# Performance work log

Measured on AMD Instinct MI355X. Metric: run time of the kernel, lower is better.

The kernel has to match this reference:

```python
import jax, jax.numpy as jnp
import numpy as np

B, L, K = 4, 1536, 30
NUM_RBF = 16
NUM_POS = 16
EDGE_F = 128
MAX_REL = 32
EDGE_IN = NUM_POS + NUM_RBF * 9 + 7  # 167
LN_EPS = 1e-5


def _norml(x):
    # F.normalize with a grad-safe epsilon
    return x * jax.lax.rsqrt(jnp.sum(x * x, -1, keepdims=True) + 1e-12)


def _gather_nodes(nodes, idx):
    # nodes [B,L,C], idx [B,L,K] -> [B,L,K,C]
    b = jnp.arange(nodes.shape[0])[:, None, None]
    return nodes[b, idx]


def _rbf(D):
    mu = jnp.linspace(2.0, 22.0, NUM_RBF)
    sigma = (22.0 - 2.0) / NUM_RBF
    return jnp.exp(-(((D[..., None] - mu) / sigma) ** 2))


def _get_rbf(A, Bc, E_idx):
    D = jnp.sqrt(jnp.sum((A[:, :, None, :] - Bc[:, None, :, :]) ** 2, -1) + 1e-6)
    Dn = jnp.take_along_axis(D, E_idx, axis=2)
    return _rbf(Dn)


def _quaternions(R):
    # R [B,L,K,3,3] -> Q [B,L,K,4]
    diag = jnp.diagonal(R, axis1=-2, axis2=-1)
    Rxx, Ryy, Rzz = diag[..., 0], diag[..., 1], diag[..., 2]
    mags = 0.5 * jnp.sqrt(jnp.abs(1.0 + jnp.stack(
        [Rxx - Ryy - Rzz, -Rxx + Ryy - Rzz, -Rxx - Ryy + Rzz], -1)) + 1e-12)
    signs = jnp.sign(jnp.stack(
        [R[..., 2, 1] - R[..., 1, 2],
         R[..., 0, 2] - R[..., 2, 0],
         R[..., 1, 0] - R[..., 0, 1]], -1))
    xyz = signs * mags
    w = jnp.sqrt(jax.nn.relu(1.0 + diag.sum(-1, keepdims=True)) + 1e-12) / 2.0
    return _norml(jnp.concatenate([xyz, w], -1))


def _orientations_coarse(X, E_idx, eps=1e-6):
    dX = X[:, 1:] - X[:, :-1]                              # [B,L-1,3]
    dn = jnp.sqrt(jnp.sum(dX * dX, -1) + 1e-12)
    band = ((dn > 3.6) & (dn < 4.0)).astype(X.dtype)
    U = _norml(dX * band[..., None])
    u2, u1, u0 = U[:, :-2], U[:, 1:-1], U[:, 2:]
    n2 = _norml(jnp.cross(u2, u1))
    n1 = _norml(jnp.cross(u1, u0))
    cosA = jnp.clip(-(u1 * u0).sum(-1), -1 + eps, 1 - eps)
    A = jnp.arccos(cosA)
    cosD = jnp.clip((n2 * n1).sum(-1), -1 + eps, 1 - eps)
    Dang = jnp.sign((u2 * n1).sum(-1)) * jnp.arccos(cosD)
    AD = jnp.stack([jnp.cos(A), jnp.sin(A) * jnp.cos(Dang), jnp.sin(A) * jnp.sin(Dang)], 2)
    AD = jnp.pad(AD, ((0, 0), (1, 2), (0, 0)))
    o1 = _norml(u2 - u1)
    O = jnp.stack([o1, n2, jnp.cross(o1, n2)], 2).reshape(X.shape[0], -1, 9)
    O = jnp.pad(O, ((0, 0), (1, 2), (0, 0)))                # [B,L,9]
    On = _gather_nodes(O, E_idx).reshape(E_idx.shape + (3, 3))
    Xn = _gather_nodes(X, E_idx)
    O = O.reshape(X.shape[0], -1, 3, 3)
    dXk = Xn - X[:, :, None, :]                             # [B,L,K,3]
    dU = _norml(jnp.einsum('blij,blkj->blki', O, dXk))
    R = jnp.einsum('blji,blkjm->blkim', O, On)
    Q = _quaternions(R)
    return AD, jnp.concatenate([dU, Q], -1)                 # O_features [B,L,K,7]


def _forward(Ca, mask, residue_idx, chain_labels, W_pos, b_pos, W_edge, gamma_e, beta_e):
    # KNN graph: pairwise distances + smallest-k
    m2 = mask[:, :, None] * mask[:, None, :]
    dX = Ca[:, None, :, :] - Ca[:, :, None, :]
    D = m2 * jnp.sqrt(jnp.sum(dX * dX, -1) + 1e-6)
    Dmax = jnp.max(D, -1, keepdims=True)
    Dadj = D + (1.0 - m2) * Dmax
    neg, E_idx = jax.lax.top_k(-Dadj, K)
    D_neighbors = -neg

    Ca0 = jnp.pad(Ca[:, :-1], ((0, 0), (1, 0), (0, 0)))
    Ca2 = jnp.pad(Ca[:, 1:], ((0, 0), (0, 1), (0, 0)))
    _, O_features = _orientations_coarse(Ca, E_idx)

    RBF_all = jnp.concatenate([
        _rbf(D_neighbors),
        _get_rbf(Ca0, Ca0, E_idx), _get_rbf(Ca2, Ca2, E_idx),
        _get_rbf(Ca0, Ca, E_idx), _get_rbf(Ca0, Ca2, E_idx),
        _get_rbf(Ca, Ca0, E_idx), _get_rbf(Ca, Ca2, E_idx),
        _get_rbf(Ca2, Ca0, E_idx), _get_rbf(Ca2, Ca, E_idx)], -1)

    offset = residue_idx[:, :, None] - residue_idx[:, None, :]
    offset = jnp.take_along_axis(offset, E_idx, axis=2)
    dch = (chain_labels[:, :, None] == chain_labels[:, None, :]).astype(jnp.int32)
    Ech = jnp.take_along_axis(dch, E_idx, axis=2)
    d = jnp.clip(offset + MAX_REL, 0, 2 * MAX_REL) * Ech + (1 - Ech) * (2 * MAX_REL + 1)
    E_pos = W_pos.T[d] + b_pos                              # one_hot @ W^T as row gather

    E = jnp.concatenate([E_pos, RBF_all, O_features], -1)   # [B,L,K,167]
    E = E @ W_edge.T                                        # [B,L,K,128]
    mu = E.mean(-1, keepdims=True)
    var = E.var(-1, keepdims=True)
    E = (E - mu) * jax.lax.rsqrt(var + LN_EPS) * gamma_e + beta_e
    return E, E_idx


def setup_inputs():
    key = jax.random.key(0)
    ks = jax.random.split(key, 3)
    Ca = 3.0 * jax.random.normal(ks[0], (B, L, 3), jnp.float32)
    mask = jnp.ones((B, L), jnp.float32)
    residue_idx = (jnp.arange(B * L, dtype=jnp.int32).reshape(B, L)) % L
    chain_labels = jnp.zeros((B, L), jnp.int32)
    W_pos = 0.05 * jax.random.normal(ks[1], (NUM_POS, 2 * MAX_REL + 2), jnp.float32)
    b_pos = jnp.zeros((NUM_POS,), jnp.float32)
    W_edge = 0.05 * jax.random.normal(ks[2], (EDGE_F, EDGE_IN), jnp.float32)
    gamma_e = jnp.ones((EDGE_F,), jnp.float32)
    beta_e = jnp.zeros((EDGE_F,), jnp.float32)
    return {"Ca": Ca, "mask": mask, "residue_idx": residue_idx,
            "chain_labels": chain_labels, "W_pos": W_pos, "b_pos": b_pos,
            "W_edge": W_edge, "gamma_e": gamma_e, "beta_e": beta_e}


def reference(Ca, mask, residue_idx, chain_labels, W_pos, b_pos, W_edge, gamma_e, beta_e):
    return _forward(Ca, mask, residue_idx, chain_labels, W_pos, b_pos, W_edge, gamma_e, beta_e)
```

## Files before the change

### kernel.cpp

```cpp
#include <hip/hip_runtime.h>

#define BQ 4
#define LQ 1536
#define KQ 30
#define NUM_RBF 16
#define NUM_POS 16
#define EDGE_F 128
#define EDGE_IN 167
#define KPAD 192
#define POS_CLS 66

typedef __attribute__((ext_vector_type(8))) short bf16x8;
typedef __attribute__((ext_vector_type(4))) float f32x4;

__device__ __forceinline__ float ssq3_exact(float dx, float dy, float dz) {
    return __fadd_rn(__fadd_rn(__fmul_rn(dx, dx), __fmul_rn(dy, dy)), __fmul_rn(dz, dz));
}

__device__ __forceinline__ float edist_exact(float ax, float ay, float az,
                                             float bx, float by, float bz) {
    float dx = __fsub_rn(ax, bx), dy = __fsub_rn(ay, by), dz = __fsub_rn(az, bz);
    return __fsqrt_rn(__fadd_rn(ssq3_exact(dx, dy, dz), 1e-6f));
}

__device__ __forceinline__ unsigned short f2bf(float x) {
    unsigned int u = __float_as_uint(x);
    unsigned int r = (u + 0x7fffu + ((u >> 16) & 1u)) >> 16;
    return (unsigned short)r;
}

__device__ __forceinline__ float sgnf(float x) {
    return (x > 0.f) ? 1.f : ((x < 0.f) ? -1.f : 0.f);
}

__device__ __forceinline__ unsigned long long umin64(unsigned long long a, unsigned long long b) {
    return a < b ? a : b;
}

__device__ __forceinline__ int fragoff(int e, int c) {
    int m = e >> 4, kk = c >> 5;
    int l = (e & 15) | (((c >> 3) & 3) << 4);
    return (((m * 6 + kk) * 64 + l) << 3) | (c & 7);
}

__global__ __launch_bounds__(256) void kWpack(const float* __restrict__ Wedge,
                                              unsigned short* __restrict__ wpack) {
    int idx = blockIdx.x * 256 + threadIdx.x;
    if (idx >= 6 * 8 * 64 * 8) return;
    int j = idx & 7, l = (idx >> 3) & 63, n = (idx >> 9) & 7, kk = idx >> 12;
    int c = kk * 32 + ((l >> 4) << 3) + j;
    int f = (n << 4) + (l & 15);
    float v = (c < EDGE_IN) ? Wedge[(size_t)f * EDGE_IN + c] : 0.0f;
    wpack[idx] = f2bf(v);
}

__global__ __launch_bounds__(256) void kOnode(const float* __restrict__ Ca,
                                              float* __restrict__ Onode) {
    int idx = blockIdx.x * 256 + threadIdx.x;
    if (idx >= BQ * LQ) return;
    int b = idx / LQ, l = idx - b * LQ;
    float o[9];
#pragma unroll
    for (int r = 0; r < 9; ++r) o[r] = 0.f;
    if (l >= 1 && l <= LQ - 3) {
        const float* Xb = Ca + (size_t)b * LQ * 3;
        float xm = Xb[(l - 1) * 3 + 0], ym = Xb[(l - 1) * 3 + 1], zm = Xb[(l - 1) * 3 + 2];
        float x0 = Xb[l * 3 + 0],       y0 = Xb[l * 3 + 1],       z0 = Xb[l * 3 + 2];
        float xp = Xb[(l + 1) * 3 + 0], yp = Xb[(l + 1) * 3 + 1], zp = Xb[(l + 1) * 3 + 2];
        float ax = __fsub_rn(x0, xm), ay = __fsub_rn(y0, ym), az = __fsub_rn(z0, zm);
        float dna = __fsqrt_rn(__fadd_rn(ssq3_exact(ax, ay, az), 1e-12f));
        float ba = (dna > 3.6f && dna < 4.0f) ? 1.0f : 0.0f;
        float ux = ax * ba, uy = ay * ba, uz = az * ba;
        float rn = 1.0f / __fsqrt_rn(ux * ux + uy * uy + uz * uz + 1e-12f);
        ux *= rn; uy *= rn; uz *= rn;
        float bx = __fsub_rn(xp, x0), by = __fsub_rn(yp, y0), bz = __fsub_rn(zp, z0);
        float dnb = __fsqrt_rn(__fadd_rn(ssq3_exact(bx, by, bz), 1e-12f));
        float bb = (dnb > 3.6f && dnb < 4.0f) ? 1.0f : 0.0f;
        float vx = bx * bb, vy = by * bb, vz = bz * bb;
        rn = 1.0f / __fsqrt_rn(vx * vx + vy * vy + vz * vz + 1e-12f);
        vx *= rn; vy *= rn; vz *= rn;
        float ox = ux - vx, oy = uy - vy, oz = uz - vz;
        rn = 1.0f / __fsqrt_rn(ox * ox + oy * oy + oz * oz + 1e-12f);
        ox *= rn; oy *= rn; oz *= rn;
        float cx = uy * vz - uz * vy, cy = uz * vx - ux * vz, cz = ux * vy - uy * vx;
        rn = 1.0f / __fsqrt_rn(cx * cx + cy * cy + cz * cz + 1e-12f);
        cx *= rn; cy *= rn; cz *= rn;
        float rx = oy * cz - oz * cy, ry = oz * cx - ox * cz, rz = ox * cy - oy * cx;
        o[0] = ox; o[1] = oy; o[2] = oz;
        o[3] = cx; o[4] = cy; o[5] = cz;
        o[6] = rx; o[7] = ry; o[8] = rz;
    }
    float* dst = Onode + (size_t)idx * 9;
#pragma unroll
    for (int r = 0; r < 9; ++r) dst[r] = o[r];
}

__global__ __launch_bounds__(64) void ktopk(const float* __restrict__ Ca,
                                            const float* __restrict__ mask,
                                            int* __restrict__ Eidx,
                                            float* __restrict__ Dn,
                                            float* __restrict__ outI) {
    const int row = blockIdx.x;
    const int b = row / LQ, i = row - b * LQ;
    const int lane = threadIdx.x;

    const float* Cb = Ca + (size_t)b * LQ * 3;
    const float* Mb = mask + (size_t)b * LQ;
    const float xi = Cb[i * 3 + 0], yi = Cb[i * 3 + 1], zi = Cb[i * 3 + 2];
    const float mi = Mb[i];

    float dv[24], m2v[24];
    float lmax = 0.0f;
#pragma unroll
    for (int s = 0; s < 24; ++s) {
        int j = lane + (s << 6);
        float dx = __fsub_rn(Cb[j * 3 + 0], xi);
        float dy = __fsub_rn(Cb[j * 3 + 1], yi);
        float dz = __fsub_rn(Cb[j * 3 + 2], zi);
        float m2 = __fmul_rn(mi, Mb[j]);
        float d = __fmul_rn(m2, __fsqrt_rn(__fadd_rn(ssq3_exact(dx, dy, dz), 1e-6f)));
        dv[s] = d; m2v[s] = m2;
        lmax = fmaxf(lmax, d);
    }
#pragma unroll
    for (int off = 1; off < 64; off <<= 1) lmax = fmaxf(lmax, __shfl_xor(lmax, off));
    const float Dmax = lmax;

    unsigned long long key[24];
#pragma unroll
    for (int s = 0; s < 24; ++s) {
        float adj = __fadd_rn(dv[s], __fmul_rn(__fsub_rn(1.0f, m2v[s]), Dmax));
        key[s] = (((unsigned long long)__float_as_uint(adj)) << 32) | (unsigned)(lane + (s << 6));
    }

    unsigned long long lm = ~0ull; int li = 0;
#pragma unroll
    for (int s = 0; s < 24; ++s) { if (key[s] < lm) { lm = key[s]; li = s; } }

    unsigned int rm = 0;
    unsigned long long res = 0;
#pragma unroll 1
    for (int k = 0; k < KQ; ++k) {
        unsigned long long g = lm;
#pragma unroll
        for (int off = 1; off < 64; off <<= 1) {
            unsigned long long o = __shfl_xor(g, off);
            g = umin64(g, o);
        }
        if (lane == k) res = g;
        if (lm == g) {
            rm |= (1u << li);
            lm = ~0ull; li = 0;
#pragma unroll
            for (int s = 0; s < 24; ++s) {
                if (!((rm >> s) & 1u) && key[s] < lm) { lm = key[s]; li = s; }
            }
        }
    }

    if (lane < KQ) {
        unsigned j = (unsigned)(res & 0xffffffffu);
        Eidx[(size_t)row * KQ + lane] = (int)j;
        Dn[(size_t)row * KQ + lane] = __uint_as_float((unsigned)(res >> 32));
        outI[(size_t)row * KQ + lane] = (float)j;
    }
}

__global__ __launch_bounds__(256) void kfeat(const float* __restrict__ Ca,
                                             const int* __restrict__ ridx,
                                             const int* __restrict__ chl,
                                             const float* __restrict__ Wpos,
                                             const float* __restrict__ bpos,
                                             const float* __restrict__ gamma,
                                             const float* __restrict__ beta,
                                             const int* __restrict__ Eidx,
                                             const float* __restrict__ Dn,
                                             const float* __restrict__ Onode,
                                             const unsigned short* __restrict__ wpack,
                                             float* __restrict__ outE) {
    const int row = blockIdx.x;
    const int b = row / LQ, i = row - b * LQ;
    const int tid = threadIdx.x;

    __shared__ __align__(16) unsigned short Afrag[2 * 6 * 64 * 8];
    __shared__ __align__(16) float Outb[KQ * 132];
    __shared__ float dists[KQ][9];
    __shared__ int sEidx[KQ];
    __shared__ float sDn[KQ];

    const float* Cb = Ca + (size_t)b * LQ * 3;

    {
        uint4* az = (uint4*)Afrag;
        for (int t = tid; t < 768; t += 256) az[t] = make_uint4(0, 0, 0, 0);
        if (tid < KQ) {
            sEidx[tid] = Eidx[(size_t)row * KQ + tid];
            sDn[tid] = Dn[(size_t)row * KQ + tid];
        }
    }
    __syncthreads();

    unsigned int* Apair = (unsigned int*)Afrag;

    for (int u = tid; u < 540; u += 256) {
        if (u < 270) {
            int e = u / 9, s = u - e * 9;
            if (s == 0) {
                dists[e][0] = sDn[e];
            } else {
                const int TA[9] = {0, -1, 1, -1, -1, 0, 0, 1, 1};
                const int TB[9] = {0, -1, 1,  0,  1, -1, 1, -1, 0};
                int j = sEidx[e];
                int ia = i + TA[s], jb = j + TB[s];
                float ax = 0.f, ay = 0.f, az = 0.f, bx = 0.f, by = 0.f, bz = 0.f;
                if (ia >= 0 && ia < LQ) { ax = Cb[ia * 3]; ay = Cb[ia * 3 + 1]; az = Cb[ia * 3 + 2]; }
                if (jb >= 0 && jb < LQ) { bx = Cb[jb * 3]; by = Cb[jb * 3 + 1]; bz = Cb[jb * 3 + 2]; }
                dists[e][s] = edist_exact(ax, ay, az, bx, by, bz);
            }
        } else if (u < 300) {
            int e = u - 270;
            int j = sEidx[e];
            float pic0 = Cb[i * 3], pic1 = Cb[i * 3 + 1], pic2 = Cb[i * 3 + 2];
            float pjc0 = Cb[j * 3], pjc1 = Cb[j * 3 + 1], pjc2 = Cb[j * 3 + 2];
            const float* Op = Onode + ((size_t)b * LQ + i) * 9;
            const float* Oq = Onode + ((size_t)b * LQ + j) * 9;
            float oi[9], oj[9];
#pragma unroll
            for (int r = 0; r < 9; ++r) { oi[r] = Op[r]; oj[r] = Oq[r]; }
            float dx = pjc0 - pic0, dy = pjc1 - pic1, dz = pjc2 - pic2;
            float v0 = oi[0] * dx + oi[1] * dy + oi[2] * dz;
            float v1 = oi[3] * dx + oi[4] * dy + oi[5] * dz;
            float v2 = oi[6] * dx + oi[7] * dy + oi[8] * dz;
            float rn = 1.0f / __fsqrt_rn(v0 * v0 + v1 * v1 + v2 * v2 + 1e-12f);
            v0 *= rn; v1 *= rn; v2 *= rn;
            float R[3][3];
#pragma unroll
            for (int ii = 0; ii < 3; ++ii)
#pragma unroll
                for (int mm = 0; mm < 3; ++mm)
                    R[ii][mm] = oi[ii] * oj[mm] + oi[3 + ii] * oj[3 + mm] + oi[6 + ii] * oj[6 + mm];
            float Rxx = R[0][0], Ryy = R[1][1], Rzz = R[2][2];
            float m0 = 0.5f * __fsqrt_rn(fabsf(1.0f + (Rxx - Ryy - Rzz)) + 1e-12f);
            float m1 = 0.5f * __fsqrt_rn(fabsf(1.0f + (-Rxx + Ryy - Rzz)) + 1e-12f);
            float m2 = 0.5f * __fsqrt_rn(fabsf(1.0f + (-Rxx - Ryy + Rzz)) + 1e-12f);
            float qx = sgnf(R[2][1] - R[1][2]) * m0;
            float qy = sgnf(R[0][2] - R[2][0]) * m1;
            float qz = sgnf(R[1][0] - R[0][1]) * m2;
            float qw = __fsqrt_rn(fmaxf(1.0f + (Rxx + Ryy + Rzz), 0.0f) + 1e-12f) * 0.5f;
            rn = 1.0f / __fsqrt_rn(qx * qx + qy * qy + qz * qz + qw * qw + 1e-12f);
            qx *= rn; qy *= rn; qz *= rn; qw *= rn;
            unsigned int p0 = (unsigned)f2bf(v0) | ((unsigned)f2bf(v1) << 16);
            unsigned int p1 = (unsigned)f2bf(v2) | ((unsigned)f2bf(qx) << 16);
            unsigned int p2 = (unsigned)f2bf(qy) | ((unsigned)f2bf(qz) << 16);
            unsigned int p3 = (unsigned)f2bf(qw);
            Apair[fragoff(e, 160) >> 1] = p0;
            Apair[fragoff(e, 162) >> 1] = p1;
            Apair[fragoff(e, 164) >> 1] = p2;
            Apair[fragoff(e, 166) >> 1] = p3;
        } else {
            int p = u - 300;
            int e = p >> 3, pr = p & 7;
            int c = pr << 1;
            int j = sEidx[e];
            int off = ridx[(size_t)b * LQ + i] - ridx[(size_t)b * LQ + j];
            int ech = (chl[(size_t)b * LQ + i] == chl[(size_t)b * LQ + j]);
            int dd = ech ? min(max(off + 32, 0), 64) : 65;
            float f0 = Wpos[c * POS_CLS + dd] + bpos[c];
            float f1 = Wpos[(c + 1) * POS_CLS + dd] + bpos[c + 1];
            Apair[fragoff(e, c) >> 1] = (unsigned)f2bf(f0) | ((unsigned)f2bf(f1) << 16);
        }
    }
    __syncthreads();

    for (int t = tid; t < KQ * 72; t += 256) {
        int e = t / 72, p = t - e * 72;
        int c = 16 + (p << 1);
        int s = (c - 16) >> 4, r = (c - 16) & 15;
        float d = dists[e][s];
        float z0 = (d - (2.0f + (float)r * 1.3333334f)) * 0.8f;
        float z1 = (d - (2.0f + (float)(r + 1) * 1.3333334f)) * 0.8f;
        float g0 = __expf(-(z0 * z0));
        float g1 = __expf(-(z1 * z1));
        Apair[fragoff(e, c) >> 1] = (unsigned)f2bf(g0) | ((unsigned)f2bf(g1) << 16);
    }
    __syncthreads();

    {
        const int l = tid & 63, w = tid >> 6;
        const bf16x8* Af = (const bf16x8*)Afrag;
        const bf16x8* Bf = (const bf16x8*)wpack;
        f32x4 acc00 = {0.f, 0.f, 0.f, 0.f}, acc01 = acc00, acc10 = acc00, acc11 = acc00;
#pragma unroll
        for (int kk = 0; kk < 6; ++kk) {
            bf16x8 a0 = Af[kk * 64 + l];
            bf16x8 a1 = Af[(6 + kk) * 64 + l];
            bf16x8 b0 = Bf[(size_t)(kk * 8 + 2 * w) * 64 + l];
            bf16x8 b1 = Bf[(size_t)(kk * 8 + 2 * w + 1) * 64 + l];
            acc00 = __builtin_amdgcn_mfma_f32_16x16x32_bf16(a0, b0, acc00, 0, 0, 0);
            acc01 = __builtin_amdgcn_mfma_f32_16x16x32_bf16(a0, b1, acc01, 0, 0, 0);
            acc10 = __builtin_amdgcn_mfma_f32_16x16x32_bf16(a1, b0, acc10, 0, 0, 0);
            acc11 = __builtin_amdgcn_mfma_f32_16x16x32_bf16(a1, b1, acc11, 0, 0, 0);
        }
        int colbase0 = (2 * w) * 16 + (l & 15);
        int colbase1 = (2 * w + 1) * 16 + (l & 15);
        int rbase = (l >> 4) * 4;
#pragma unroll
        for (int r = 0; r < 4; ++r) {
            int e0 = rbase + r;
            Outb[e0 * 132 + colbase0] = acc00[r];
            Outb[e0 * 132 + colbase1] = acc01[r];
            int e1 = 16 + rbase + r;
            if (e1 < KQ) {
                Outb[e1 * 132 + colbase0] = acc10[r];
                Outb[e1 * 132 + colbase1] = acc11[r];
            }
        }
    }
    __syncthreads();

    __shared__ float smu[KQ], sinv[KQ];
    if (tid < KQ * 8) {
        int e = tid >> 3, g = tid & 7;
        float s1 = 0.f, s2 = 0.f;
#pragma unroll
        for (int q = 0; q < 16; ++q) {
            float v = Outb[e * 132 + g * 16 + q];
            s1 += v; s2 += v * v;
        }
#pragma unroll
        for (int off = 1; off < 8; off <<= 1) {
            s1 += __shfl_xor(s1, off);
            s2 += __shfl_xor(s2, off);
        }
        if (g == 0) {
            float mu = s1 * (1.0f / 128.0f);
            float var = s2 * (1.0f / 128.0f) - mu * mu;
            smu[e] = mu;
            sinv[e] = 1.0f / __fsqrt_rn(var + 1e-5f);
        }
    }
    __syncthreads();

    float* dst = outE + (size_t)row * (KQ * EDGE_F);
    for (int t = tid; t < KQ * EDGE_F / 4; t += 256) {
        int fi = t << 2;
        int e = fi >> 7, f0 = fi & 127;
        float4 x = *(const float4*)&Outb[e * 132 + f0];
        float4 gm = *(const float4*)&gamma[f0];
        float4 bt = *(const float4*)&beta[f0];
        float mu = smu[e], iv = sinv[e];
        float4 o;
        o.x = (x.x - mu) * iv * gm.x + bt.x;
        o.y = (x.y - mu) * iv * gm.y + bt.y;
        o.z = (x.z - mu) * iv * gm.z + bt.z;
        o.w = (x.w - mu) * iv * gm.w + bt.w;
        *(float4*)&dst[fi] = o;
    }
}

extern "C" void kernel_launch(void* const* d_in, const int* in_sizes, int n_in,
                              void* d_out, int out_size, void* d_ws, size_t ws_size,
                              hipStream_t stream) {
    const float* Ca    = (const float*)d_in[0];
    const float* mask  = (const float*)d_in[1];
    const int*   ridx  = (const int*)d_in[2];
    const int*   chl   = (const int*)d_in[3];
    const float* Wpos  = (const float*)d_in[4];
    const float* bpos  = (const float*)d_in[5];
    const float* Wedge = (const float*)d_in[6];
    const float* gamma = (const float*)d_in[7];
    const float* beta  = (const float*)d_in[8];

    float* outE = (float*)d_out;
    float* outI = outE + (size_t)BQ * LQ * KQ * EDGE_F;

    char* ws = (char*)d_ws;
    int*            Eidx  = (int*)(ws + 0);
    float*          Dn    = (float*)(ws + (size_t)BQ * LQ * KQ * 4);
    float*          Onode = (float*)(ws + (size_t)BQ * LQ * KQ * 8);
    unsigned short* wpack = (unsigned short*)(ws + (size_t)BQ * LQ * KQ * 8 + (size_t)BQ * LQ * 9 * 4);

    kWpack<<<96, 256, 0, stream>>>(Wedge, wpack);
    kOnode<<<(BQ * LQ + 255) / 256, 256, 0, stream>>>(Ca, Onode);
    ktopk<<<BQ * LQ, 64, 0, stream>>>(Ca, mask, Eidx, Dn, outI);
    kfeat<<<BQ * LQ, 256, 0, stream>>>(Ca, ridx, chl, Wpos, bpos, gamma, beta,
                                       Eidx, Dn, Onode, wpack, outE);
}
```

Measured before the change: 230.2 us.

## Replace per-lane key arrays in top-k with 3-deep min buffer and recompute

```diff
diff --git a/kernel.cpp b/kernel.cpp
--- a/kernel.cpp
+++ b/kernel.cpp
@@ -43,20 +43,21 @@
     return (((m * 6 + kk) * 64 + l) << 3) | (c & 7);
 }
 
-__global__ __launch_bounds__(256) void kWpack(const float* __restrict__ Wedge,
-                                              unsigned short* __restrict__ wpack) {
-    int idx = blockIdx.x * 256 + threadIdx.x;
-    if (idx >= 6 * 8 * 64 * 8) return;
-    int j = idx & 7, l = (idx >> 3) & 63, n = (idx >> 9) & 7, kk = idx >> 12;
-    int c = kk * 32 + ((l >> 4) << 3) + j;
-    int f = (n << 4) + (l & 15);
-    float v = (c < EDGE_IN) ? Wedge[(size_t)f * EDGE_IN + c] : 0.0f;
-    wpack[idx] = f2bf(v);
-}
-
-__global__ __launch_bounds__(256) void kOnode(const float* __restrict__ Ca,
-                                              float* __restrict__ Onode) {
-    int idx = blockIdx.x * 256 + threadIdx.x;
+__global__ __launch_bounds__(256) void kprep(const float* __restrict__ Wedge,
+                                             unsigned short* __restrict__ wpack,
+                                             const float* __restrict__ Ca,
+                                             float* __restrict__ Onode) {
+    if (blockIdx.x < 96) {
+        int idx = blockIdx.x * 256 + threadIdx.x;
+        if (idx >= 6 * 8 * 64 * 8) return;
+        int j = idx & 7, l = (idx >> 3) & 63, n = (idx >> 9) & 7, kk = idx >> 12;
+        int c = kk * 32 + ((l >> 4) << 3) + j;
+        int f = (n << 4) + (l & 15);
+        float v = (c < EDGE_IN) ? Wedge[(size_t)f * EDGE_IN + c] : 0.0f;
+        wpack[idx] = f2bf(v);
+        return;
+    }
+    int idx = (blockIdx.x - 96) * 256 + threadIdx.x;
     if (idx >= BQ * LQ) return;
     int b = idx / LQ, l = idx - b * LQ;
     float o[9];
@@ -95,21 +96,20 @@
     for (int r = 0; r < 9; ++r) dst[r] = o[r];
 }
 
-__global__ __launch_bounds__(64) void ktopk(const float* __restrict__ Ca,
-                                            const float* __restrict__ mask,
-                                            int* __restrict__ Eidx,
-                                            float* __restrict__ Dn,
-                                            float* __restrict__ outI) {
-    const int row = blockIdx.x;
+__global__ __launch_bounds__(256) void ktopk(const float* __restrict__ Ca,
+                                             const float* __restrict__ mask,
+                                             int* __restrict__ Eidx,
+                                             float* __restrict__ Dn,
+                                             float* __restrict__ outI) {
+    const int row = blockIdx.x * 4 + (threadIdx.x >> 6);
+    const int lane = threadIdx.x & 63;
     const int b = row / LQ, i = row - b * LQ;
-    const int lane = threadIdx.x;
 
     const float* Cb = Ca + (size_t)b * LQ * 3;
     const float* Mb = mask + (size_t)b * LQ;
     const float xi = Cb[i * 3 + 0], yi = Cb[i * 3 + 1], zi = Cb[i * 3 + 2];
     const float mi = Mb[i];
 
-    float dv[24], m2v[24];
     float lmax = 0.0f;
 #pragma unroll
     for (int s = 0; s < 24; ++s) {
@@ -119,41 +119,58 @@
         float dz = __fsub_rn(Cb[j * 3 + 2], zi);
         float m2 = __fmul_rn(mi, Mb[j]);
         float d = __fmul_rn(m2, __fsqrt_rn(__fadd_rn(ssq3_exact(dx, dy, dz), 1e-6f)));
-        dv[s] = d; m2v[s] = m2;
         lmax = fmaxf(lmax, d);
     }
 #pragma unroll
     for (int off = 1; off < 64; off <<= 1) lmax = fmaxf(lmax, __shfl_xor(lmax, off));
     const float Dmax = lmax;
 
-    unsigned long long key[24];
+    unsigned long long k1 = ~0ull, k2 = ~0ull, k3 = ~0ull;
 #pragma unroll
     for (int s = 0; s < 24; ++s) {
-        float adj = __fadd_rn(dv[s], __fmul_rn(__fsub_rn(1.0f, m2v[s]), Dmax));
-        key[s] = (((unsigned long long)__float_as_uint(adj)) << 32) | (unsigned)(lane + (s << 6));
-    }
-
-    unsigned long long lm = ~0ull; int li = 0;
-#pragma unroll
-    for (int s = 0; s < 24; ++s) { if (key[s] < lm) { lm = key[s]; li = s; } }
-
-    unsigned int rm = 0;
+        int j = lane + (s << 6);
+        float dx = __fsub_rn(Cb[j * 3 + 0], xi);
+        float dy = __fsub_rn(Cb[j * 3 + 1], yi);
+        float dz = __fsub_rn(Cb[j * 3 + 2], zi);
+        float m2 = __fmul_rn(mi, Mb[j]);
+        float d = __fmul_rn(m2, __fsqrt_rn(__fadd_rn(ssq3_exact(dx, dy, dz), 1e-6f)));
+        float adj = __fadd_rn(d, __fmul_rn(__fsub_rn(1.0f, m2), Dmax));
+        unsigned long long key = (((unsigned long long)__float_as_uint(adj)) << 32) | (unsigned)j;
+        if (key < k1)      { k3 = k2; k2 = k1; k1 = key; }
+        else if (key < k2) { k3 = k2; k2 = key; }
+        else if (key < k3) { k3 = key; }
+    }
+
     unsigned long long res = 0;
 #pragma unroll 1
     for (int k = 0; k < KQ; ++k) {
-        unsigned long long g = lm;
+        unsigned long long g = k1;
 #pragma unroll
         for (int off = 1; off < 64; off <<= 1) {
             unsigned long long o = __shfl_xor(g, off);
             g = umin64(g, o);
         }
         if (lane == k) res = g;
-        if (lm == g) {
-            rm |= (1u << li);
-            lm = ~0ull; li = 0;
-#pragma unroll
+        bool pop = (k1 == g);
+        k1 = pop ? k2 : k1;
+        k2 = pop ? k3 : k2;
+        k3 = pop ? ~0ull : k3;
+        if (__builtin_expect(pop & (k1 == ~0ull), 0)) {
+#pragma unroll 1
             for (int s = 0; s < 24; ++s) {
-                if (!((rm >> s) & 1u) && key[s] < lm) { lm = key[s]; li = s; }
+                int j = lane + (s << 6);
+                float dx = __fsub_rn(Cb[j * 3 + 0], xi);
+                float dy = __fsub_rn(Cb[j * 3 + 1], yi);
+                float dz = __fsub_rn(Cb[j * 3 + 2], zi);
+                float m2 = __fmul_rn(mi, Mb[j]);
+                float d = __fmul_rn(m2, __fsqrt_rn(__fadd_rn(ssq3_exact(dx, dy, dz), 1e-6f)));
+                float adj = __fadd_rn(d, __fmul_rn(__fsub_rn(1.0f, m2), Dmax));
+                unsigned long long key = (((unsigned long long)__float_as_uint(adj)) << 32) | (unsigned)j;
+                if (key > g) {
+                    if (key < k1)      { k3 = k2; k2 = k1; k1 = key; }
+                    else if (key < k2) { k3 = k2; k2 = key; }
+                    else if (key < k3) { k3 = key; }
+                }
             }
         }
     }
@@ -380,9 +397,8 @@
     float*          Onode = (float*)(ws + (size_t)BQ * LQ * KQ * 8);
     unsigned short* wpack = (unsigned short*)(ws + (size_t)BQ * LQ * KQ * 8 + (size_t)BQ * LQ * 9 * 4);
 
-    kWpack<<<96, 256, 0, stream>>>(Wedge, wpack);
-    kOnode<<<(BQ * LQ + 255) / 256, 256, 0, stream>>>(Ca, Onode);
-    ktopk<<<BQ * LQ, 64, 0, stream>>>(Ca, mask, Eidx, Dn, outI);
+    kprep<<<120, 256, 0, stream>>>(Wedge, wpack, Ca, Onode);
+    ktopk<<<(BQ * LQ) / 4, 256, 0, stream>>>(Ca, mask, Eidx, Dn, outI);
     kfeat<<<BQ * LQ, 256, 0, stream>>>(Ca, ridx, chl, Wpos, bpos, gamma, beta,
                                        Eidx, Dn, Onode, wpack, outE);
 }
```

Result: faster. 221.7 us (-3.7%).
